# Optimization experiments

Measured on AMD Instinct MI355X. Metric: run time of the kernel, lower is better.

The kernel has to match this reference:

```python
import jax, jax.numpy as jnp
import numpy as np

N_NODES = 200000
D_FEAT = 512
B = 512
S1, S2 = 25, 10  # num_samples for layer 0 and layer 1
HID = 256
NUM_CLASSES = 50


def setup_inputs() -> dict:
    key = jax.random.key(0)
    ks = jax.random.split(key, 10)
    sc = 0.05
    return {
        "features": jax.random.normal(ks[0], (N_NODES, D_FEAT), jnp.float32),
        "W_self0": jax.random.normal(ks[1], (D_FEAT, HID), jnp.float32) * sc,
        "W_neigh0": jax.random.normal(ks[2], (D_FEAT, HID), jnp.float32) * sc,
        "W_self1": jax.random.normal(ks[3], (2 * HID, HID), jnp.float32) * sc,
        "W_neigh1": jax.random.normal(ks[4], (2 * HID, HID), jnp.float32) * sc,
        "W_pred": jax.random.normal(ks[5], (2 * HID, NUM_CLASSES), jnp.float32) * sc,
        "b_pred": jnp.zeros((NUM_CLASSES,), jnp.float32),
        "samples0": jax.random.randint(ks[6], (B,), 0, N_NODES, jnp.int64 if jax.config.read('jax_enable_x64') else jnp.int32),
        "samples1": jax.random.randint(ks[7], (B * S2,), 0, N_NODES, jnp.int64 if jax.config.read('jax_enable_x64') else jnp.int32),
        "samples2": jax.random.randint(ks[8], (B * S2 * S1,), 0, N_NODES, jnp.int64 if jax.config.read('jax_enable_x64') else jnp.int32),
    }


def _mean_agg(h_self, h_neigh, W_self, W_neigh, act):
    # h_self: [n, d_in]; h_neigh: [n, S, d_in]
    neigh_mean = h_neigh.mean(axis=1)
    out = jnp.concatenate([h_self @ W_self, neigh_mean @ W_neigh], axis=-1)
    return act(out)


def reference(features, W_self0, W_neigh0, W_self1, W_neigh1, W_pred, b_pred,
              samples0, samples1, samples2):
    # irregular gathers of the support tree
    h0 = features[samples0]                      # [B, d]
    h1 = features[samples1]                      # [B*S2, d]
    h2 = features[samples2]                      # [B*S2*S1, d]
    # layer 0 (relu, dim_mult=1): applied at hops 0 and 1
    n0 = _mean_agg(h0, h1.reshape(B, S2, D_FEAT), W_self0, W_neigh0, jax.nn.relu)          # [B, 2H]
    n1 = _mean_agg(h1, h2.reshape(B * S2, S1, D_FEAT), W_self0, W_neigh0, jax.nn.relu)     # [B*S2, 2H]
    # layer 1 (identity act, dim_mult=2)
    out = _mean_agg(n0, n1.reshape(B, S2, 2 * HID), W_self1, W_neigh1, lambda x: x)        # [B, 2H]
    # F.normalize(p=2, dim=1), eps=1e-12
    norm = out / jnp.maximum(jnp.linalg.norm(out, axis=1, keepdims=True), 1e-12)
    logits = norm @ W_pred + b_pred
    return logits
```

## Files before the change

### kernel.cpp

```cpp
#include <hip/hip_runtime.h>

#define DF   512
#define HID2 512
#define NHID 256
#define NCLS 50
#define NB   512

typedef __attribute__((ext_vector_type(8))) short short8;
typedef __attribute__((ext_vector_type(4))) float float4v;

__device__ __forceinline__ float b2f(unsigned short u) {
    union { unsigned int i; float f; } v; v.i = ((unsigned int)u) << 16; return v.f;
}
__device__ __forceinline__ unsigned short f2b(float f) {
    union { float f; unsigned int u; } v; v.f = f;
    unsigned int r = v.u + 0x7FFFu + ((v.u >> 16) & 1u);
    return (unsigned short)(r >> 16);
}
__device__ __forceinline__ float blo(unsigned int u) {
    union { unsigned int i; float f; } v; v.i = u << 16; return v.f;
}
__device__ __forceinline__ float bhi(unsigned int u) {
    union { unsigned int i; float f; } v; v.i = u & 0xFFFF0000u; return v.f;
}
__device__ __forceinline__ unsigned int pk2(float a, float b) {
    return (unsigned int)f2b(a) | ((unsigned int)f2b(b) << 16);
}

__global__ __launch_bounds__(256) void preprocess(
        const float* __restrict__ feat,
        const float* __restrict__ W0, const float* __restrict__ W1,
        const float* __restrict__ W2, const float* __restrict__ W3,
        unsigned short* __restrict__ Wt,
        const int* __restrict__ s0, const int* __restrict__ s1,
        const int* __restrict__ s2,
        unsigned short* __restrict__ h0bf, unsigned short* __restrict__ h1bf,
        unsigned short* __restrict__ h1mean, unsigned short* __restrict__ h2mean) {
    __shared__ unsigned short T[64][66];
    const int b = blockIdx.x;
    const int t = threadIdx.x;

    if (b >= 2816 && b < 2944) {
        const int w = b - 2816;
        const int x = w & 7, y = (w >> 3) & 3, z = w >> 5;
        const float* W = (z == 0) ? W0 : (z == 1) ? W1 : (z == 2) ? W2 : W3;
        unsigned short* Out = Wt + (size_t)z * NHID * DF;
        const int k0 = x * 64, n0 = y * 64;
#pragma unroll
        for (int p = 0; p < 4; ++p) {
            const int k = p * 16 + (t >> 4);
            const int n = (t & 15) * 4;
            const float4 v = *(const float4*)(W + (size_t)(k0 + k) * NHID + n0 + n);
            T[n + 0][k] = f2b(v.x);
            T[n + 1][k] = f2b(v.y);
            T[n + 2][k] = f2b(v.z);
            T[n + 3][k] = f2b(v.w);
        }
        __syncthreads();
#pragma unroll
        for (int p = 0; p < 4; ++p) {
            const int n = p * 16 + (t >> 4);
            const int k = (t & 15) * 4;
            ushort4 o;
            o.x = T[n][k]; o.y = T[n][k + 1]; o.z = T[n][k + 2]; o.w = T[n][k + 3];
            *(ushort4*)(Out + (size_t)(n0 + n) * DF + k0 + k) = o;
        }
        return;
    }

    const int sub = t >> 7;
    const int col = (t & 127) * 4;

    if (b < 2560) {
        const int g = b * 2 + sub;
        float ax = 0.f, ay = 0.f, az = 0.f, aw = 0.f;
#pragma unroll
        for (int j = 0; j < 25; ++j) {
            const float4 v = *(const float4*)(feat + (size_t)s2[g * 25 + j] * DF + col);
            ax += v.x; ay += v.y; az += v.z; aw += v.w;
        }
        const float inv = 1.f / 25.f;
        ushort4 o;
        o.x = f2b(ax * inv); o.y = f2b(ay * inv);
        o.z = f2b(az * inv); o.w = f2b(aw * inv);
        *(ushort4*)(h2mean + (size_t)g * DF + col) = o;
        return;
    }
    if (b < 2816) {
        const int g = (b - 2560) * 2 + sub;
        float ax = 0.f, ay = 0.f, az = 0.f, aw = 0.f;
#pragma unroll
        for (int j = 0; j < 10; ++j) {
            const float4 v = *(const float4*)(feat + (size_t)s1[g * 10 + j] * DF + col);
            ax += v.x; ay += v.y; az += v.z; aw += v.w;
        }
        ushort4 o;
        o.x = f2b(ax * 0.1f); o.y = f2b(ay * 0.1f);
        o.z = f2b(az * 0.1f); o.w = f2b(aw * 0.1f);
        *(ushort4*)(h1mean + (size_t)g * DF + col) = o;
        return;
    }
    if (b < 3200) {
        const int r = (b - 2944) * 2 + sub;
        const float4 v = *(const float4*)(feat + (size_t)s0[r] * DF + col);
        ushort4 o; o.x = f2b(v.x); o.y = f2b(v.y); o.z = f2b(v.z); o.w = f2b(v.w);
        *(ushort4*)(h0bf + (size_t)r * DF + col) = o;
        return;
    }
    {
        const int r = (b - 3200) * 2 + sub;
        const float4 v = *(const float4*)(feat + (size_t)s1[r] * DF + col);
        ushort4 o; o.x = f2b(v.x); o.y = f2b(v.y); o.z = f2b(v.z); o.w = f2b(v.w);
        *(ushort4*)(h1bf + (size_t)r * DF + col) = o;
    }
}

__global__ __launch_bounds__(256) void gemm_fused01(
        const unsigned short* __restrict__ A1a, const unsigned short* __restrict__ A2a,
        const unsigned short* __restrict__ A1b, const unsigned short* __restrict__ A2b,
        const unsigned short* __restrict__ W1t, const unsigned short* __restrict__ W2t,
        unsigned short* __restrict__ C1, unsigned short* __restrict__ C2) {
    __shared__ unsigned short As[64][72];
    __shared__ unsigned short Bs[64][72];
    const int tid = threadIdx.x;
    const int wave = tid >> 6;
    const int lane = tid & 63;
    const bool second = (blockIdx.y >= 80);
    const int m0 = (second ? (blockIdx.y - 80) : blockIdx.y) * 64;
    const int nb = blockIdx.x * 64;
    const unsigned short* A1 = second ? A1b : A1a;
    const unsigned short* A2 = second ? A2b : A2a;
    unsigned short* C = second ? C2 : C1;
    const unsigned short* A  = (nb < 256) ? A1 : A2;
    const unsigned short* Wt = (nb < 256) ? W1t : W2t;
    const int n0 = nb & 255;

    const int sr = tid >> 3;
    const int sk = (tid & 7) * 8;

    float4v acc[4];
#pragma unroll
    for (int i = 0; i < 4; ++i) acc[i] = (float4v)(0.f);

    const int am = wave * 16 + (lane & 15);
    const int kq = (lane >> 4) * 8;

    for (int k0 = 0; k0 < DF; k0 += 64) {
        *(uint4*)&As[sr][sk]      = *(const uint4*)(A  + (size_t)(m0 + sr) * DF + k0 + sk);
        *(uint4*)&As[sr + 32][sk] = *(const uint4*)(A  + (size_t)(m0 + sr + 32) * DF + k0 + sk);
        *(uint4*)&Bs[sr][sk]      = *(const uint4*)(Wt + (size_t)(n0 + sr) * DF + k0 + sk);
        *(uint4*)&Bs[sr + 32][sk] = *(const uint4*)(Wt + (size_t)(n0 + sr + 32) * DF + k0 + sk);
        __syncthreads();
#pragma unroll
        for (int ks = 0; ks < 64; ks += 32) {
            const short8 af = *(const short8*)&As[am][ks + kq];
#pragma unroll
            for (int nt = 0; nt < 4; ++nt) {
                const short8 bf = *(const short8*)&Bs[nt * 16 + (lane & 15)][ks + kq];
                acc[nt] = __builtin_amdgcn_mfma_f32_16x16x32_bf16(af, bf, acc[nt], 0, 0, 0);
            }
        }
        __syncthreads();
    }

#pragma unroll
    for (int nt = 0; nt < 4; ++nt) {
        const int gcol = nb + nt * 16 + (lane & 15);
#pragma unroll
        for (int r = 0; r < 4; ++r) {
            const int grow = m0 + wave * 16 + (lane >> 4) * 4 + r;
            const float v = fmaxf(acc[nt][r], 0.f);
            C[(size_t)grow * HID2 + gcol] = f2b(v);
        }
    }
}

__global__ __launch_bounds__(256) void gemm_final(
        const unsigned short* __restrict__ n0rows,
        const unsigned short* __restrict__ n1rows,
        const unsigned short* __restrict__ W1t, const unsigned short* __restrict__ W2t,
        float* __restrict__ Cout) {
    __shared__ unsigned short As[64][72];
    __shared__ unsigned short Bs[64][72];
    const int tid = threadIdx.x;
    const int wave = tid >> 6;
    const int lane = tid & 63;
    const int m0 = blockIdx.y * 64;
    const int nb = blockIdx.x * 64;
    const bool meanpath = (nb >= 256);
    const unsigned short* Wt = meanpath ? W2t : W1t;
    const int n0 = nb & 255;

    const int sr = tid >> 3;
    const int sk = (tid & 7) * 8;

    float4v acc[4];
#pragma unroll
    for (int i = 0; i < 4; ++i) acc[i] = (float4v)(0.f);

    const int am = wave * 16 + (lane & 15);
    const int kq = (lane >> 4) * 8;

    for (int k0 = 0; k0 < DF; k0 += 64) {
        if (!meanpath) {
            *(uint4*)&As[sr][sk]      = *(const uint4*)(n0rows + (size_t)(m0 + sr) * DF + k0 + sk);
            *(uint4*)&As[sr + 32][sk] = *(const uint4*)(n0rows + (size_t)(m0 + sr + 32) * DF + k0 + sk);
        } else {
#pragma unroll
            for (int h = 0; h < 2; ++h) {
                const int r = sr + h * 32;
                const size_t gbase = (size_t)(m0 + r) * 10;
                float a0 = 0.f, a1 = 0.f, a2 = 0.f, a3 = 0.f;
                float a4 = 0.f, a5 = 0.f, a6 = 0.f, a7 = 0.f;
#pragma unroll
                for (int j = 0; j < 10; ++j) {
                    const uint4 v = *(const uint4*)(n1rows + (gbase + j) * DF + k0 + sk);
                    a0 += blo(v.x); a1 += bhi(v.x);
                    a2 += blo(v.y); a3 += bhi(v.y);
                    a4 += blo(v.z); a5 += bhi(v.z);
                    a6 += blo(v.w); a7 += bhi(v.w);
                }
                uint4 o;
                o.x = pk2(a0 * 0.1f, a1 * 0.1f);
                o.y = pk2(a2 * 0.1f, a3 * 0.1f);
                o.z = pk2(a4 * 0.1f, a5 * 0.1f);
                o.w = pk2(a6 * 0.1f, a7 * 0.1f);
                *(uint4*)&As[r][sk] = o;
            }
        }
        *(uint4*)&Bs[sr][sk]      = *(const uint4*)(Wt + (size_t)(n0 + sr) * DF + k0 + sk);
        *(uint4*)&Bs[sr + 32][sk] = *(const uint4*)(Wt + (size_t)(n0 + sr + 32) * DF + k0 + sk);
        __syncthreads();
#pragma unroll
        for (int ks = 0; ks < 64; ks += 32) {
            const short8 af = *(const short8*)&As[am][ks + kq];
#pragma unroll
            for (int nt = 0; nt < 4; ++nt) {
                const short8 bf = *(const short8*)&Bs[nt * 16 + (lane & 15)][ks + kq];
                acc[nt] = __builtin_amdgcn_mfma_f32_16x16x32_bf16(af, bf, acc[nt], 0, 0, 0);
            }
        }
        __syncthreads();
    }

#pragma unroll
    for (int nt = 0; nt < 4; ++nt) {
        const int gcol = nb + nt * 16 + (lane & 15);
#pragma unroll
        for (int r = 0; r < 4; ++r) {
            const int grow = m0 + wave * 16 + (lane >> 4) * 4 + r;
            Cout[(size_t)grow * HID2 + gcol] = acc[nt][r];
        }
    }
}

__global__ __launch_bounds__(256) void normalize_pred(
        const float* __restrict__ outb,
        const float* __restrict__ Wp,
        const float* __restrict__ bp,
        float* __restrict__ logits) {
    __shared__ float row[HID2];
    __shared__ float red[256];
    __shared__ float part[4][64];
    const int r = blockIdx.x;
    const int t = threadIdx.x;
    const float2 v = *(const float2*)(outb + (size_t)r * HID2 + t * 2);
    row[t * 2] = v.x;
    row[t * 2 + 1] = v.y;
    red[t] = v.x * v.x + v.y * v.y;
    __syncthreads();
    for (int s = 128; s > 0; s >>= 1) {
        if (t < s) red[t] += red[t + s];
        __syncthreads();
    }
    const float scale = 1.0f / fmaxf(sqrtf(red[0]), 1e-12f);
    const int c = t & 63;
    const int q = t >> 6;
    float acc = 0.f;
    if (c < NCLS) {
#pragma unroll 4
        for (int k = q * 128; k < q * 128 + 128; ++k) acc += row[k] * Wp[k * NCLS + c];
    }
    part[q][c] = acc;
    __syncthreads();
    if (t < NCLS) {
        logits[r * NCLS + t] =
            (part[0][t] + part[1][t] + part[2][t] + part[3][t]) * scale + bp[t];
    }
}

extern "C" void kernel_launch(void* const* d_in, const int* in_sizes, int n_in,
                              void* d_out, int out_size, void* d_ws, size_t ws_size,
                              hipStream_t stream) {
    const float* feat    = (const float*)d_in[0];
    const float* Wself0  = (const float*)d_in[1];
    const float* Wneigh0 = (const float*)d_in[2];
    const float* Wself1  = (const float*)d_in[3];
    const float* Wneigh1 = (const float*)d_in[4];
    const float* Wpred   = (const float*)d_in[5];
    const float* bpred   = (const float*)d_in[6];
    const int* s0 = (const int*)d_in[7];
    const int* s1 = (const int*)d_in[8];
    const int* s2 = (const int*)d_in[9];

    unsigned short* u = (unsigned short*)d_ws;
    unsigned short* h2mean = u;
    unsigned short* h1bf   = h2mean + 5120 * 512;
    unsigned short* n1     = h1bf   + 5120 * 512;
    unsigned short* h1mean = n1     + 5120 * 512;
    unsigned short* h0bf   = h1mean + 512 * 512;
    unsigned short* n1mean = h0bf   + 512 * 512;
    unsigned short* n0     = n1mean + 512 * 512;
    unsigned short* Wt     = n0     + 512 * 512;
    float* outb = (float*)(Wt + 4 * NHID * DF);
    unsigned short* Wt_s0 = Wt;
    unsigned short* Wt_n0 = Wt + 1 * NHID * DF;
    unsigned short* Wt_s1 = Wt + 2 * NHID * DF;
    unsigned short* Wt_n1 = Wt + 3 * NHID * DF;

    preprocess<<<5760, 256, 0, stream>>>(feat, Wself0, Wneigh0, Wself1, Wneigh1, Wt,
                                         s0, s1, s2, h0bf, h1bf, h1mean, h2mean);
    gemm_fused01<<<dim3(8, 88), 256, 0, stream>>>(h1bf, h2mean, h0bf, h1mean,
                                                  Wt_s0, Wt_n0, n1, n0);
    gemm_final<<<dim3(8, 8), 256, 0, stream>>>(n0, n1, Wt_s1, Wt_n1, outb);
    normalize_pred<<<NB, 256, 0, stream>>>(outb, Wpred, bpred, (float*)d_out);
}
```

Measured before the change: 549.4 us.

## Fuse tail GEMMs and normalize into one persistent kernel with grid barriers

Replaces the layer-0 GEMM, layer-1 GEMM and normalize/predict kernels with a single kernel of 704 blocks that synchronizes between phases using atomic-counter grid barriers. Shared memory for the GEMM and normalize phases is unioned, and the barrier counters are reset by the preprocess kernel. The aim is to remove launch overhead and tail gaps between the small dependent kernels. This relies on all 704 blocks being co-resident; otherwise the barriers deadlock. The spin-waits and fences add their own cost.

```diff
diff --git a/kernel.cpp b/kernel.cpp
--- a/kernel.cpp
+++ b/kernel.cpp
@@ -5,6 +5,7 @@
 #define NHID 256
 #define NCLS 50
 #define NB   512
+#define TAIL_BLOCKS 704u
 
 typedef __attribute__((ext_vector_type(8))) short short8;
 typedef __attribute__((ext_vector_type(4))) float float4v;
@@ -25,6 +26,19 @@
 }
 __device__ __forceinline__ unsigned int pk2(float a, float b) {
     return (unsigned int)f2b(a) | ((unsigned int)f2b(b) << 16);
+}
+
+__device__ __forceinline__ void gbar(unsigned int* ctr, unsigned int target) {
+    __syncthreads();
+    __threadfence();
+    if (threadIdx.x == 0) {
+        __hip_atomic_fetch_add(ctr, 1u, __ATOMIC_RELEASE, __HIP_MEMORY_SCOPE_AGENT);
+        while (__hip_atomic_load(ctr, __ATOMIC_ACQUIRE, __HIP_MEMORY_SCOPE_AGENT) < target) {
+            __builtin_amdgcn_s_sleep(8);
+        }
+    }
+    __syncthreads();
+    __threadfence();
 }
 
 __global__ __launch_bounds__(256) void preprocess(
@@ -35,10 +49,13 @@
         const int* __restrict__ s0, const int* __restrict__ s1,
         const int* __restrict__ s2,
         unsigned short* __restrict__ h0bf, unsigned short* __restrict__ h1bf,
-        unsigned short* __restrict__ h1mean, unsigned short* __restrict__ h2mean) {
+        unsigned short* __restrict__ h1mean, unsigned short* __restrict__ h2mean,
+        unsigned int* __restrict__ bars) {
     __shared__ unsigned short T[64][66];
     const int b = blockIdx.x;
     const int t = threadIdx.x;
+
+    if (b == 0 && t == 0) { bars[0] = 0u; bars[1] = 0u; }
 
     if (b >= 2816 && b < 2944) {
         const int w = b - 2816;
@@ -115,177 +132,172 @@
     }
 }
 
-__global__ __launch_bounds__(256) void gemm_fused01(
-        const unsigned short* __restrict__ A1a, const unsigned short* __restrict__ A2a,
-        const unsigned short* __restrict__ A1b, const unsigned short* __restrict__ A2b,
-        const unsigned short* __restrict__ W1t, const unsigned short* __restrict__ W2t,
-        unsigned short* __restrict__ C1, unsigned short* __restrict__ C2) {
-    __shared__ unsigned short As[64][72];
-    __shared__ unsigned short Bs[64][72];
+__global__ __launch_bounds__(256, 3) void fused_tail(
+        const unsigned short* __restrict__ h1bf, const unsigned short* __restrict__ h2mean,
+        const unsigned short* __restrict__ h0bf, const unsigned short* __restrict__ h1mean,
+        const unsigned short* __restrict__ Wt_s0, const unsigned short* __restrict__ Wt_n0,
+        const unsigned short* __restrict__ Wt_s1, const unsigned short* __restrict__ Wt_n1,
+        unsigned short* __restrict__ n1, unsigned short* __restrict__ n0rows,
+        float* __restrict__ outb,
+        const float* __restrict__ Wp, const float* __restrict__ bp,
+        float* __restrict__ logits,
+        unsigned int* __restrict__ bars) {
+    __shared__ union {
+        struct { unsigned short As[64][72]; unsigned short Bs[64][72]; } g;
+        struct { float row[HID2]; float red[256]; float part[4][64]; } nz;
+    } sm;
+
+    const int bid = blockIdx.x;
     const int tid = threadIdx.x;
     const int wave = tid >> 6;
     const int lane = tid & 63;
-    const bool second = (blockIdx.y >= 80);
-    const int m0 = (second ? (blockIdx.y - 80) : blockIdx.y) * 64;
-    const int nb = blockIdx.x * 64;
-    const unsigned short* A1 = second ? A1b : A1a;
-    const unsigned short* A2 = second ? A2b : A2a;
-    unsigned short* C = second ? C2 : C1;
-    const unsigned short* A  = (nb < 256) ? A1 : A2;
-    const unsigned short* Wt = (nb < 256) ? W1t : W2t;
-    const int n0 = nb & 255;
-
     const int sr = tid >> 3;
     const int sk = (tid & 7) * 8;
-
-    float4v acc[4];
-#pragma unroll
-    for (int i = 0; i < 4; ++i) acc[i] = (float4v)(0.f);
-
     const int am = wave * 16 + (lane & 15);
     const int kq = (lane >> 4) * 8;
 
-    for (int k0 = 0; k0 < DF; k0 += 64) {
-        *(uint4*)&As[sr][sk]      = *(const uint4*)(A  + (size_t)(m0 + sr) * DF + k0 + sk);
-        *(uint4*)&As[sr + 32][sk] = *(const uint4*)(A  + (size_t)(m0 + sr + 32) * DF + k0 + sk);
-        *(uint4*)&Bs[sr][sk]      = *(const uint4*)(Wt + (size_t)(n0 + sr) * DF + k0 + sk);
-        *(uint4*)&Bs[sr + 32][sk] = *(const uint4*)(Wt + (size_t)(n0 + sr + 32) * DF + k0 + sk);
+    {
+        const int xb = bid & 7;
+        const int yb = bid >> 3;
+        const bool second = (yb >= 80);
+        const int m0 = (second ? (yb - 80) : yb) * 64;
+        const int nb = xb * 64;
+        const unsigned short* A1 = second ? h0bf : h1bf;
+        const unsigned short* A2 = second ? h1mean : h2mean;
+        unsigned short* C = second ? n0rows : n1;
+        const unsigned short* A  = (nb < 256) ? A1 : A2;
+        const unsigned short* Wt = (nb < 256) ? Wt_s0 : Wt_n0;
+        const int n0 = nb & 255;
+
+        float4v acc[4];
+#pragma unroll
+        for (int i = 0; i < 4; ++i) acc[i] = (float4v)(0.f);
+
+        for (int k0 = 0; k0 < DF; k0 += 64) {
+            *(uint4*)&sm.g.As[sr][sk]      = *(const uint4*)(A  + (size_t)(m0 + sr) * DF + k0 + sk);
+            *(uint4*)&sm.g.As[sr + 32][sk] = *(const uint4*)(A  + (size_t)(m0 + sr + 32) * DF + k0 + sk);
+            *(uint4*)&sm.g.Bs[sr][sk]      = *(const uint4*)(Wt + (size_t)(n0 + sr) * DF + k0 + sk);
+            *(uint4*)&sm.g.Bs[sr + 32][sk] = *(const uint4*)(Wt + (size_t)(n0 + sr + 32) * DF + k0 + sk);
+            __syncthreads();
+#pragma unroll
+            for (int ks = 0; ks < 64; ks += 32) {
+                const short8 af = *(const short8*)&sm.g.As[am][ks + kq];
+#pragma unroll
+                for (int nt = 0; nt < 4; ++nt) {
+                    const short8 bf = *(const short8*)&sm.g.Bs[nt * 16 + (lane & 15)][ks + kq];
+                    acc[nt] = __builtin_amdgcn_mfma_f32_16x16x32_bf16(af, bf, acc[nt], 0, 0, 0);
+                }
+            }
+            __syncthreads();
+        }
+
+#pragma unroll
+        for (int nt = 0; nt < 4; ++nt) {
+            const int gcol = nb + nt * 16 + (lane & 15);
+#pragma unroll
+            for (int r = 0; r < 4; ++r) {
+                const int grow = m0 + wave * 16 + (lane >> 4) * 4 + r;
+                const float v = fmaxf(acc[nt][r], 0.f);
+                C[(size_t)grow * HID2 + gcol] = f2b(v);
+            }
+        }
+    }
+
+    gbar(&bars[0], TAIL_BLOCKS);
+
+    if (bid < 64) {
+        const int xb = bid & 7;
+        const int m0 = (bid >> 3) * 64;
+        const int nb = xb * 64;
+        const bool meanpath = (nb >= 256);
+        const unsigned short* Wt = meanpath ? Wt_n1 : Wt_s1;
+        const int n0 = nb & 255;
+
+        float4v acc[4];
+#pragma unroll
+        for (int i = 0; i < 4; ++i) acc[i] = (float4v)(0.f);
+
+        for (int k0 = 0; k0 < DF; k0 += 64) {
+            if (!meanpath) {
+                *(uint4*)&sm.g.As[sr][sk]      = *(const uint4*)(n0rows + (size_t)(m0 + sr) * DF + k0 + sk);
+                *(uint4*)&sm.g.As[sr + 32][sk] = *(const uint4*)(n0rows + (size_t)(m0 + sr + 32) * DF + k0 + sk);
+            } else {
+#pragma unroll
+                for (int h = 0; h < 2; ++h) {
+                    const int r = sr + h * 32;
+                    const size_t gbase = (size_t)(m0 + r) * 10;
+                    float a0 = 0.f, a1 = 0.f, a2 = 0.f, a3 = 0.f;
+                    float a4 = 0.f, a5 = 0.f, a6 = 0.f, a7 = 0.f;
+#pragma unroll
+                    for (int j = 0; j < 10; ++j) {
+                        const uint4 v = *(const uint4*)(n1 + (gbase + j) * DF + k0 + sk);
+                        a0 += blo(v.x); a1 += bhi(v.x);
+                        a2 += blo(v.y); a3 += bhi(v.y);
+                        a4 += blo(v.z); a5 += bhi(v.z);
+                        a6 += blo(v.w); a7 += bhi(v.w);
+                    }
+                    uint4 o;
+                    o.x = pk2(a0 * 0.1f, a1 * 0.1f);
+                    o.y = pk2(a2 * 0.1f, a3 * 0.1f);
+                    o.z = pk2(a4 * 0.1f, a5 * 0.1f);
+                    o.w = pk2(a6 * 0.1f, a7 * 0.1f);
+                    *(uint4*)&sm.g.As[r][sk] = o;
+                }
+            }
+            *(uint4*)&sm.g.Bs[sr][sk]      = *(const uint4*)(Wt + (size_t)(n0 + sr) * DF + k0 + sk);
+            *(uint4*)&sm.g.Bs[sr + 32][sk] = *(const uint4*)(Wt + (size_t)(n0 + sr + 32) * DF + k0 + sk);
+            __syncthreads();
+#pragma unroll
+            for (int ks = 0; ks < 64; ks += 32) {
+                const short8 af = *(const short8*)&sm.g.As[am][ks + kq];
+#pragma unroll
+                for (int nt = 0; nt < 4; ++nt) {
+                    const short8 bf = *(const short8*)&sm.g.Bs[nt * 16 + (lane & 15)][ks + kq];
+                    acc[nt] = __builtin_amdgcn_mfma_f32_16x16x32_bf16(af, bf, acc[nt], 0, 0, 0);
+                }
+            }
+            __syncthreads();
+        }
+
+#pragma unroll
+        for (int nt = 0; nt < 4; ++nt) {
+            const int gcol = nb + nt * 16 + (lane & 15);
+#pragma unroll
+            for (int r = 0; r < 4; ++r) {
+                const int grow = m0 + wave * 16 + (lane >> 4) * 4 + r;
+                outb[(size_t)grow * HID2 + gcol] = acc[nt][r];
+            }
+        }
+    }
+
+    gbar(&bars[1], TAIL_BLOCKS);
+
+    if (bid < NB) {
+        const int r = bid;
+        const int t = tid;
+        const float2 v = *(const float2*)(outb + (size_t)r * HID2 + t * 2);
+        sm.nz.row[t * 2] = v.x;
+        sm.nz.row[t * 2 + 1] = v.y;
+        sm.nz.red[t] = v.x * v.x + v.y * v.y;
         __syncthreads();
-#pragma unroll
-        for (int ks = 0; ks < 64; ks += 32) {
-            const short8 af = *(const short8*)&As[am][ks + kq];
-#pragma unroll
-            for (int nt = 0; nt < 4; ++nt) {
-                const short8 bf = *(const short8*)&Bs[nt * 16 + (lane & 15)][ks + kq];
-                acc[nt] = __builtin_amdgcn_mfma_f32_16x16x32_bf16(af, bf, acc[nt], 0, 0, 0);
-            }
-        }
+        for (int s = 128; s > 0; s >>= 1) {
+            if (t < s) sm.nz.red[t] += sm.nz.red[t + s];
+            __syncthreads();
+        }
+        const float scale = 1.0f / fmaxf(sqrtf(sm.nz.red[0]), 1e-12f);
+        const int c = t & 63;
+        const int q = t >> 6;
+        float acc = 0.f;
+        if (c < NCLS) {
+#pragma unroll 4
+            for (int k = q * 128; k < q * 128 + 128; ++k) acc += sm.nz.row[k] * Wp[k * NCLS + c];
+        }
+        sm.nz.part[q][c] = acc;
         __syncthreads();
-    }
-
-#pragma unroll
-    for (int nt = 0; nt < 4; ++nt) {
-        const int gcol = nb + nt * 16 + (lane & 15);
-#pragma unroll
-        for (int r = 0; r < 4; ++r) {
-            const int grow = m0 + wave * 16 + (lane >> 4) * 4 + r;
-            const float v = fmaxf(acc[nt][r], 0.f);
-            C[(size_t)grow * HID2 + gcol] = f2b(v);
-        }
-    }
-}
-
-__global__ __launch_bounds__(256) void gemm_final(
-        const unsigned short* __restrict__ n0rows,
-        const unsigned short* __restrict__ n1rows,
-        const unsigned short* __restrict__ W1t, const unsigned short* __restrict__ W2t,
-        float* __restrict__ Cout) {
-    __shared__ unsigned short As[64][72];
-    __shared__ unsigned short Bs[64][72];
-    const int tid = threadIdx.x;
-    const int wave = tid >> 6;
-    const int lane = tid & 63;
-    const int m0 = blockIdx.y * 64;
-    const int nb = blockIdx.x * 64;
-    const bool meanpath = (nb >= 256);
-    const unsigned short* Wt = meanpath ? W2t : W1t;
-    const int n0 = nb & 255;
-
-    const int sr = tid >> 3;
-    const int sk = (tid & 7) * 8;
-
-    float4v acc[4];
-#pragma unroll
-    for (int i = 0; i < 4; ++i) acc[i] = (float4v)(0.f);
-
-    const int am = wave * 16 + (lane & 15);
-    const int kq = (lane >> 4) * 8;
-
-    for (int k0 = 0; k0 < DF; k0 += 64) {
-        if (!meanpath) {
-            *(uint4*)&As[sr][sk]      = *(const uint4*)(n0rows + (size_t)(m0 + sr) * DF + k0 + sk);
-            *(uint4*)&As[sr + 32][sk] = *(const uint4*)(n0rows + (size_t)(m0 + sr + 32) * DF + k0 + sk);
-        } else {
-#pragma unroll
-            for (int h = 0; h < 2; ++h) {
-                const int r = sr + h * 32;
-                const size_t gbase = (size_t)(m0 + r) * 10;
-                float a0 = 0.f, a1 = 0.f, a2 = 0.f, a3 = 0.f;
-                float a4 = 0.f, a5 = 0.f, a6 = 0.f, a7 = 0.f;
-#pragma unroll
-                for (int j = 0; j < 10; ++j) {
-                    const uint4 v = *(const uint4*)(n1rows + (gbase + j) * DF + k0 + sk);
-                    a0 += blo(v.x); a1 += bhi(v.x);
-                    a2 += blo(v.y); a3 += bhi(v.y);
-                    a4 += blo(v.z); a5 += bhi(v.z);
-                    a6 += blo(v.w); a7 += bhi(v.w);
-                }
-                uint4 o;
-                o.x = pk2(a0 * 0.1f, a1 * 0.1f);
-                o.y = pk2(a2 * 0.1f, a3 * 0.1f);
-                o.z = pk2(a4 * 0.1f, a5 * 0.1f);
-                o.w = pk2(a6 * 0.1f, a7 * 0.1f);
-                *(uint4*)&As[r][sk] = o;
-            }
-        }
-        *(uint4*)&Bs[sr][sk]      = *(const uint4*)(Wt + (size_t)(n0 + sr) * DF + k0 + sk);
-        *(uint4*)&Bs[sr + 32][sk] = *(const uint4*)(Wt + (size_t)(n0 + sr + 32) * DF + k0 + sk);
-        __syncthreads();
-#pragma unroll
-        for (int ks = 0; ks < 64; ks += 32) {
-            const short8 af = *(const short8*)&As[am][ks + kq];
-#pragma unroll
-            for (int nt = 0; nt < 4; ++nt) {
-                const short8 bf = *(const short8*)&Bs[nt * 16 + (lane & 15)][ks + kq];
-                acc[nt] = __builtin_amdgcn_mfma_f32_16x16x32_bf16(af, bf, acc[nt], 0, 0, 0);
-            }
-        }
-        __syncthreads();
-    }
-
-#pragma unroll
-    for (int nt = 0; nt < 4; ++nt) {
-        const int gcol = nb + nt * 16 + (lane & 15);
-#pragma unroll
-        for (int r = 0; r < 4; ++r) {
-            const int grow = m0 + wave * 16 + (lane >> 4) * 4 + r;
-            Cout[(size_t)grow * HID2 + gcol] = acc[nt][r];
-        }
-    }
-}
-
-__global__ __launch_bounds__(256) void normalize_pred(
-        const float* __restrict__ outb,
-        const float* __restrict__ Wp,
-        const float* __restrict__ bp,
-        float* __restrict__ logits) {
-    __shared__ float row[HID2];
-    __shared__ float red[256];
-    __shared__ float part[4][64];
-    const int r = blockIdx.x;
-    const int t = threadIdx.x;
-    const float2 v = *(const float2*)(outb + (size_t)r * HID2 + t * 2);
-    row[t * 2] = v.x;
-    row[t * 2 + 1] = v.y;
-    red[t] = v.x * v.x + v.y * v.y;
-    __syncthreads();
-    for (int s = 128; s > 0; s >>= 1) {
-        if (t < s) red[t] += red[t + s];
-        __syncthreads();
-    }
-    const float scale = 1.0f / fmaxf(sqrtf(red[0]), 1e-12f);
-    const int c = t & 63;
-    const int q = t >> 6;
-    float acc = 0.f;
-    if (c < NCLS) {
-#pragma unroll 4
-        for (int k = q * 128; k < q * 128 + 128; ++k) acc += row[k] * Wp[k * NCLS + c];
-    }
-    part[q][c] = acc;
-    __syncthreads();
-    if (t < NCLS) {
-        logits[r * NCLS + t] =
-            (part[0][t] + part[1][t] + part[2][t] + part[3][t]) * scale + bp[t];
+        if (t < NCLS) {
+            logits[r * NCLS + t] =
+                (sm.nz.part[0][t] + sm.nz.part[1][t] + sm.nz.part[2][t] + sm.nz.part[3][t]) * scale + bp[t];
+        }
     }
 }
 
@@ -313,15 +325,16 @@
     unsigned short* n0     = n1mean + 512 * 512;
     unsigned short* Wt     = n0     + 512 * 512;
     float* outb = (float*)(Wt + 4 * NHID * DF);
+    unsigned int* bars = (unsigned int*)(outb + 512 * 512);
     unsigned short* Wt_s0 = Wt;
     unsigned short* Wt_n0 = Wt + 1 * NHID * DF;
     unsigned short* Wt_s1 = Wt + 2 * NHID * DF;
     unsigned short* Wt_n1 = Wt + 3 * NHID * DF;
 
     preprocess<<<5760, 256, 0, stream>>>(feat, Wself0, Wneigh0, Wself1, Wneigh1, Wt,
-                                         s0, s1, s2, h0bf, h1bf, h1mean, h2mean);
-    gemm_fused01<<<dim3(8, 88), 256, 0, stream>>>(h1bf, h2mean, h0bf, h1mean,
-                                                  Wt_s0, Wt_n0, n1, n0);
-    gemm_final<<<dim3(8, 8), 256, 0, stream>>>(n0, n1, Wt_s1, Wt_n1, outb);
-    normalize_pred<<<NB, 256, 0, stream>>>(outb, Wpred, bpred, (float*)d_out);
-}
+                                         s0, s1, s2, h0bf, h1bf, h1mean, h2mean, bars);
+    fused_tail<<<TAIL_BLOCKS, 256, 0, stream>>>(h1bf, h2mean, h0bf, h1mean,
+                                                Wt_s0, Wt_n0, Wt_s1, Wt_n1,
+                                                n1, n0, outb, Wpred, bpred,
+                                                (float*)d_out, bars);
+}
```

New measurement: 1.033 ms. 1.88x slower.
